# Performance work log

Measured on AMD Instinct MI355X. Metric: run time of the kernel, lower is better.

## Reference

```python
import jax, jax.numpy as jnp
import numpy as np

B, D, C, N = 8, 49, 512, 12
BN_EPS = 1e-5
SCALE = (C // 2) ** -0.5


def bn_train(x, axes):
    # training-mode batchnorm, gamma=1 beta=0 (per bn_init / default init)
    m = jnp.mean(x, axis=axes, keepdims=True)
    v = jnp.var(x, axis=axes, keepdims=True)
    return (x - m) * jax.lax.rsqrt(v + BN_EPS)


def l2norm(x):
    n = jnp.linalg.norm(x, axis=-1, keepdims=True)
    return x / jnp.maximum(n, 1e-12)


def cross_attn(y, xkv, wq, bq, wk, bk, wv, bv):
    q = y @ wq + bq
    k = xkv @ wk + bk
    v = xkv @ wv + bv
    a = jax.nn.softmax(jnp.einsum('...ik,...jk->...ij', q, k) * SCALE, axis=-1)
    return a @ v


def _gnn_layer(xv, ed, wa, wb, we, wu, wv):
    # incidence-matrix einsums reduce to repeat (end-gather) / tile (start-gather)
    res = xv
    agg = jnp.repeat(xv @ wa, N, axis=1) + jnp.tile(xv @ wb, (1, N, 1)) + ed @ we
    ed = ed + jax.nn.relu(bn_train(agg, (0, 2)))
    e = jax.nn.sigmoid(ed).reshape(-1, N, N, C)
    e = jax.nn.softmax(e, axis=2).reshape(-1, N * N, C)
    uj = jnp.tile(xv @ wv, (1, N, 1))
    msg = (e * uj).reshape(-1, N, N, C).sum(axis=2) / N  # scatter via end.T
    xv = jax.nn.relu(res + bn_train(xv @ wu + msg, (0, 2)))
    return xv, ed


def setup_inputs() -> dict:
    ks = iter(jax.random.split(jax.random.key(0), 64))

    def nrm(shape, scale=0.02):
        return jax.random.normal(next(ks), shape, dtype=jnp.float32) * scale

    g = float(np.sqrt(2.0 / C))
    inp = {'x': jax.random.normal(next(ks), (B, D, C), dtype=jnp.float32)}
    inp['Wc'] = nrm((N, C, C))
    inp['bc'] = nrm((N, C), 0.01)
    for p in ('fam', 'arm'):
        inp[p + '_wq'] = nrm((C, C // 2))
        inp[p + '_bq'] = nrm((C // 2,), 0.01)
        inp[p + '_wk'] = nrm((C, C // 2))
        inp[p + '_bk'] = nrm((C // 2,), 0.01)
        inp[p + '_wv'] = nrm((C, C))
        inp[p + '_bv'] = nrm((C,), 0.01)
    inp['ep_w'] = nrm((C, C))
    inp['ep_b'] = nrm((C,), 0.01)
    for nm in ('g_wa1', 'g_wb1', 'g_we1', 'g_wu1', 'g_wv1',
               'g_wa2', 'g_wb2', 'g_we2', 'g_wu2', 'g_wv2'):
        inp[nm] = nrm((C, C), g)
    inp['sc'] = nrm((N, C), float(np.sqrt(6.0 / (N + C))))
    inp['efc_w'] = nrm((C, 4), float(np.sqrt(6.0 / (C + 4))))
    inp['efc_b'] = nrm((4,), 0.01)
    return inp


def reference(x, Wc, bc,
              fam_wq, fam_bq, fam_wk, fam_bk, fam_wv, fam_bv,
              arm_wq, arm_bq, arm_wk, arm_bk, arm_wv, arm_bv,
              ep_w, ep_b,
              g_wa1, g_wb1, g_we1, g_wu1, g_wv1,
              g_wa2, g_wb2, g_we2, g_wu2, g_wv2,
              sc, efc_w, efc_b):
    b = x.shape[0]
    # per-class LinearBlocks (fc -> BN -> ReLU), vectorized over classes
    h = jnp.einsum('bdc,nco->bndo', x, Wc) + bc[None, :, None, :]
    f_u = jax.nn.relu(bn_train(h, (0, 2)))          # (b, N, D, C)
    f_v = f_u.mean(axis=2)                           # (b, N, C)
    # GEM edge extractor
    gf = jnp.broadcast_to(x[:, None], (b, N, D, C))
    feat = cross_attn(f_u, gf, fam_wq, fam_bq, fam_wk, fam_bk, fam_wv, fam_bv)
    feat_end = jnp.repeat(feat, N, axis=1)           # (b, N*N, D, C): edge (i,j) -> node i
    feat_start = jnp.tile(feat, (1, N, 1, 1))        # edge (i,j) -> node j
    feat = cross_attn(feat_start, feat_end, arm_wq, arm_bq, arm_wk, arm_bk, arm_wv, arm_bv)
    f_e = bn_train(feat @ ep_w + ep_b, (0, 2, 3)).mean(axis=2)  # (b, N*N, C)
    # cosine-similarity adjacency mask (detached), digraph-normalized
    si = l2norm(jax.lax.stop_gradient(f_v))
    adj = jnp.einsum('bik,bjk->bij', si, si)
    dis = jnp.sum(adj, axis=-1) ** -0.5
    mask = (adj * dis[:, :, None] * dis[:, None, :]).reshape(b, N * N, 1)
    f_e = f_e * mask
    # two GNN message-passing layers
    f_v, f_e = _gnn_layer(f_v, f_e, g_wa1, g_wb1, g_we1, g_wu1, g_wv1)
    f_v, f_e = _gnn_layer(f_v, f_e, g_wa2, g_wb2, g_we2, g_wu2, g_wv2)
    # cosine classifier + edge fc
    scn = l2norm(jax.nn.relu(sc))
    cl = jnp.sum(l2norm(f_v) * scn[None], axis=-1)   # (b, N)
    cl_edge = f_e @ efc_w + efc_b                    # (b, N*N, 4)
    return cl, cl_edge
```

## Files before the change

kernel.cpp:

```cpp
#include <hip/hip_runtime.h>
#include <math.h>

namespace {

constexpr int B = 8, D = 49, C = 512, N = 12, H = 256, E = 144;
constexpr int M_BD  = B * D;
constexpr int M_BND = B * N * D;
constexpr float BN_EPS = 1e-5f;
constexpr float ATT_SCALE = 0.0625f;

typedef __attribute__((ext_vector_type(4))) float  floatx4;
typedef __attribute__((ext_vector_type(8))) short  shortx8;

__device__ inline unsigned short f2bf(float f) {
  unsigned u = __float_as_uint(f);
  return (unsigned short)((u + 0x7fffu + ((u >> 16) & 1u)) >> 16);
}
__device__ inline float bf2f(unsigned short u) {
  return __uint_as_float(((unsigned)u) << 16);
}

__device__ inline void gload16(const unsigned short* g, unsigned short* l) {
  __builtin_amdgcn_global_load_lds(
      (const __attribute__((address_space(1))) void*)g,
      (__attribute__((address_space(3))) void*)l, 16, 0, 0);
}

struct TCJobs {
  const float* src[28];
  unsigned short* dst[28];
  int nn[28];
};

__global__ __launch_bounds__(256)
void tcast_k(TCJobs jobs,
             const float* __restrict__ x, unsigned short* __restrict__ xb,
             const float* __restrict__ awv, unsigned short* __restrict__ armwvb,
             const float* __restrict__ bk, const float* __restrict__ bv,
             const float* __restrict__ bq2, const float* __restrict__ bk2,
             const float* __restrict__ arm_bv, const float* __restrict__ epw,
             const float* __restrict__ epb,
             float* __restrict__ kvbias, float* __restrict__ qkvbias)
{
  const int z = blockIdx.z;
  const int tid = threadIdx.x;
  if (z == 28) {
    int idx = (blockIdx.y * 16 + blockIdx.x) * 256 + tid;
    const int n1 = M_BD * C / 8;
    const int n2 = n1 + C * C / 8;
    if (idx < n1) {
      int i8 = idx * 8;
      float4 a = *reinterpret_cast<const float4*>(x + i8);
      float4 b = *reinterpret_cast<const float4*>(x + i8 + 4);
      shortx8 o;
      o[0]=(short)f2bf(a.x); o[1]=(short)f2bf(a.y); o[2]=(short)f2bf(a.z); o[3]=(short)f2bf(a.w);
      o[4]=(short)f2bf(b.x); o[5]=(short)f2bf(b.y); o[6]=(short)f2bf(b.z); o[7]=(short)f2bf(b.w);
      *reinterpret_cast<shortx8*>(xb + i8) = o;
    } else if (idx < n2) {
      int i8 = (idx - n1) * 8;
      float4 a = *reinterpret_cast<const float4*>(awv + i8);
      float4 b = *reinterpret_cast<const float4*>(awv + i8 + 4);
      shortx8 o;
      o[0]=(short)f2bf(a.x); o[1]=(short)f2bf(a.y); o[2]=(short)f2bf(a.z); o[3]=(short)f2bf(a.w);
      o[4]=(short)f2bf(b.x); o[5]=(short)f2bf(b.y); o[6]=(short)f2bf(b.z); o[7]=(short)f2bf(b.w);
      *reinterpret_cast<shortx8*>(armwvb + i8) = o;
    } else if (idx >= 58112 && idx < 58624) {
      int c = idx - 58112;
      float s = epb[c];
      for (int k = 0; k < C; ++k) s = fmaf(arm_bv[k], epw[k * C + c], s);
      qkvbias[512 + c] = s;
    }
    if (idx < 256) { kvbias[idx] = bk[idx]; qkvbias[idx] = bq2[idx]; qkvbias[256 + idx] = bk2[idx]; }
    if (idx < 512) kvbias[256 + idx] = bv[idx];
    return;
  }
  const float* src = jobs.src[z];
  unsigned short* dst = jobs.dst[z];
  const int Nn = jobs.nn[z];
  const int tx = blockIdx.x, ty = blockIdx.y;
  if (tx * 32 >= Nn) return;
  __shared__ float t[32][33];
  const int lr = tid >> 5, lc = tid & 31;
#pragma unroll
  for (int p = 0; p < 4; ++p) {
    int k = ty * 32 + p * 8 + lr;
    t[p * 8 + lr][lc] = src[(long long)k * Nn + tx * 32 + lc];
  }
  __syncthreads();
#pragma unroll
  for (int p = 0; p < 4; ++p) {
    int n = tx * 32 + p * 8 + lr;
    dst[(long long)n * 512 + ty * 32 + lc] = f2bf(t[lc][p * 8 + lr]);
  }
}

__device__ __forceinline__
void gemm64_body(const void* __restrict__ Ain, const unsigned short* __restrict__ Bt,
                 const float* __restrict__ bp, float* __restrict__ co,
                 unsigned short* __restrict__ cb,
                 int M, int Nn, int K, int lda, int ldb, int ldc, int abf,
                 int bx, int by)
{
  const float* Af = abf ? nullptr : (const float*)Ain;
  const unsigned short* Ab = abf ? (const unsigned short*)Ain : nullptr;

  __shared__ short As[64 * 72];
  __shared__ short Bs[64 * 72];

  const int tid = threadIdx.x;
  const int row0 = bx * 64, col0 = by * 64;
  const int wid = tid >> 6, lane = tid & 63;
  const int wr = wid >> 1, wc = wid & 1;
  const int lr = lane & 15, lg = lane >> 4;

  floatx4 acc00 = {0.f,0.f,0.f,0.f}, acc01 = {0.f,0.f,0.f,0.f};
  floatx4 acc10 = {0.f,0.f,0.f,0.f}, acc11 = {0.f,0.f,0.f,0.f};

  const int r = tid >> 2, seg = tid & 3;
  const int gr = row0 + r, gn = col0 + r;
  short* aw = &As[r * 72 + seg * 16];
  short* bw = &Bs[r * 72 + seg * 16];
  const shortx8 zz = {0,0,0,0,0,0,0,0};

  for (int k0 = 0; k0 < K; k0 += 64) {
    shortx8 w0, w1;
    if (gr < M) {
      if (abf) {
        const shortx8* ap = reinterpret_cast<const shortx8*>(Ab + (long long)gr * lda + seg * 16 + k0);
        w0 = ap[0]; w1 = ap[1];
      } else {
        const float4* ap = reinterpret_cast<const float4*>(Af + (long long)gr * lda + seg * 16 + k0);
        float4 fa0 = ap[0], fa1 = ap[1], fa2 = ap[2], fa3 = ap[3];
        w0[0]=(short)f2bf(fa0.x); w0[1]=(short)f2bf(fa0.y); w0[2]=(short)f2bf(fa0.z); w0[3]=(short)f2bf(fa0.w);
        w0[4]=(short)f2bf(fa1.x); w0[5]=(short)f2bf(fa1.y); w0[6]=(short)f2bf(fa1.z); w0[7]=(short)f2bf(fa1.w);
        w1[0]=(short)f2bf(fa2.x); w1[1]=(short)f2bf(fa2.y); w1[2]=(short)f2bf(fa2.z); w1[3]=(short)f2bf(fa2.w);
        w1[4]=(short)f2bf(fa3.x); w1[5]=(short)f2bf(fa3.y); w1[6]=(short)f2bf(fa3.z); w1[7]=(short)f2bf(fa3.w);
      }
    } else { w0 = zz; w1 = zz; }
    const shortx8* bp8 = reinterpret_cast<const shortx8*>(Bt + (long long)gn * ldb + seg * 16 + k0);
    shortx8 b0v = bp8[0];
    shortx8 b1v = bp8[1];

    __syncthreads();
    *reinterpret_cast<shortx8*>(aw)     = w0;
    *reinterpret_cast<shortx8*>(aw + 8) = w1;
    *reinterpret_cast<shortx8*>(bw)     = b0v;
    *reinterpret_cast<shortx8*>(bw + 8) = b1v;
    __syncthreads();

#pragma unroll
    for (int kt = 0; kt < 2; ++kt) {
      shortx8 a0 = *reinterpret_cast<const shortx8*>(&As[(wr*32      + lr) * 72 + kt*32 + lg*8]);
      shortx8 a1 = *reinterpret_cast<const shortx8*>(&As[(wr*32 + 16 + lr) * 72 + kt*32 + lg*8]);
      shortx8 bb0 = *reinterpret_cast<const shortx8*>(&Bs[(wc*32      + lr) * 72 + kt*32 + lg*8]);
      shortx8 bb1 = *reinterpret_cast<const shortx8*>(&Bs[(wc*32 + 16 + lr) * 72 + kt*32 + lg*8]);
      acc00 = __builtin_amdgcn_mfma_f32_16x16x32_bf16(a0, bb0, acc00, 0, 0, 0);
      acc01 = __builtin_amdgcn_mfma_f32_16x16x32_bf16(a0, bb1, acc01, 0, 0, 0);
      acc10 = __builtin_amdgcn_mfma_f32_16x16x32_bf16(a1, bb0, acc10, 0, 0, 0);
      acc11 = __builtin_amdgcn_mfma_f32_16x16x32_bf16(a1, bb1, acc11, 0, 0, 0);
    }
  }

  const int colA = col0 + wc * 32 + lr;
  const int colB = colA + 16;
  const bool okA = colA < Nn, okB = colB < Nn;
  const float biasA = (bp && okA) ? bp[colA] : 0.f;
  const float biasB = (bp && okB) ? bp[colB] : 0.f;
  const int rb0 = row0 + wr * 32 + lg * 4;
  const int rb1 = rb0 + 16;
#pragma unroll
  for (int jj = 0; jj < 4; ++jj) {
    int ra = rb0 + jj, rb = rb1 + jj;
    float v00 = acc00[jj] + biasA, v01 = acc01[jj] + biasB;
    float v10 = acc10[jj] + biasA, v11 = acc11[jj] + biasB;
    if (ra < M) {
      if (co) { if (okA) co[(long long)ra * ldc + colA] = v00;
                if (okB) co[(long long)ra * ldc + colB] = v01; }
      if (cb) { if (okA) cb[(long long)ra * ldc + colA] = f2bf(v00);
                if (okB) cb[(long long)ra * ldc + colB] = f2bf(v01); }
    }
    if (rb < M) {
      if (co) { if (okA) co[(long long)rb * ldc + colA] = v10;
                if (okB) co[(long long)rb * ldc + colB] = v11; }
      if (cb) { if (okA) cb[(long long)rb * ldc + colA] = f2bf(v10);
                if (okB) cb[(long long)rb * ldc + colB] = f2bf(v11); }
    }
  }
}

__global__ __launch_bounds__(256)
void gemm_mfma(const void* __restrict__ Ain, const unsigned short* __restrict__ Bt,
               const float* __restrict__ bias, float* __restrict__ Co,
               unsigned short* __restrict__ Cb,
               int M, int Nn, int K, int lda, int ldb, int ldc, int abf,
               long long sA, long long sB, long long sBias, long long sC)
{
  const int z = blockIdx.z;
  const void* A = abf ? (const void*)((const unsigned short*)Ain + z * sA)
                      : (const void*)((const float*)Ain + z * sA);
  gemm64_body(A, Bt + z * sB, bias ? bias + z * sBias : nullptr,
              Co ? Co + z * sC : nullptr, Cb ? Cb + z * sC : nullptr,
              M, Nn, K, lda, ldb, ldc, abf, blockIdx.x, blockIdx.y);
}

struct GJob {
  const void* A; const unsigned short* B; const float* bias;
  float* Co; unsigned short* Cb;
  int M, Nn, K, lda, ldb, ldc, abf, tx;
};
struct GJobs { GJob j[3]; int ends[3]; int n; };

__global__ __launch_bounds__(256)
void gemm_jobs(GJobs js)
{
  const int bid = blockIdx.x;
#pragma unroll
  for (int q = 0; q < 3; ++q) {
    if (q < js.n && bid < js.ends[q]) {
      int start = q ? js.ends[q - 1] : 0;
      int local = bid - start;
      const GJob& J = js.j[q];
      gemm64_body(J.A, J.B, J.bias, J.Co, J.Cb,
                  J.M, J.Nn, J.K, J.lda, J.ldb, J.ldc, J.abf,
                  local % J.tx, local / J.tx);
      return;
    }
  }
}

__device__ __forceinline__
void g128_body(const unsigned short* __restrict__ Ab, const unsigned short* __restrict__ Bt,
               const float* __restrict__ bp, float* __restrict__ co,
               unsigned short* __restrict__ cb, float* __restrict__ psb, float* __restrict__ pqb,
               int M, int Nn, int K, int lda, int ldb, int ldc, int bx, int by)
{
  __shared__ unsigned short As[128 * 64];
  __shared__ unsigned short Bs[128 * 64];

  const int tid = threadIdx.x;
  const int row0 = bx * 128, col0 = by * 128;
  const int wid = tid >> 6, lane = tid & 63;
  const int wr = wid >> 1, wc = wid & 1;
  const int lr = lane & 15, lg = lane >> 4;

  floatx4 acc[4][4];
#pragma unroll
  for (int mf = 0; mf < 4; ++mf)
#pragma unroll
    for (int nf = 0; nf < 4; ++nf) acc[mf][nf] = floatx4{0.f,0.f,0.f,0.f};

  const int rsub = tid >> 3;
  const int csub = (tid & 7) * 8;

  for (int k0 = 0; k0 < K; k0 += 64) {
    __syncthreads();
#pragma unroll
    for (int it = 0; it < 4; ++it) {
      int r = it * 32 + rsub;
      gload16(Ab + (long long)(row0 + r) * lda + k0 + csub, As + it * 2048 + tid * 8);
      gload16(Bt + (long long)(col0 + r) * ldb + k0 + csub, Bs + it * 2048 + tid * 8);
    }
    __syncthreads();

#pragma unroll
    for (int kt = 0; kt < 2; ++kt) {
      shortx8 af[4], bf[4];
#pragma unroll
      for (int mf = 0; mf < 4; ++mf)
        af[mf] = *reinterpret_cast<const shortx8*>(&As[(wr*64 + mf*16 + lr) * 64 + kt*32 + lg*8]);
#pragma unroll
      for (int nf = 0; nf < 4; ++nf)
        bf[nf] = *reinterpret_cast<const shortx8*>(&Bs[(wc*64 + nf*16 + lr) * 64 + kt*32 + lg*8]);
#pragma unroll
      for (int mf = 0; mf < 4; ++mf)
#pragma unroll
        for (int nf = 0; nf < 4; ++nf)
          acc[mf][nf] = __builtin_amdgcn_mfma_f32_16x16x32_bf16(af[mf], bf[nf], acc[mf][nf], 0, 0, 0);
    }
  }

#pragma unroll
  for (int nf = 0; nf < 4; ++nf) {
    const int col = col0 + wc * 64 + nf * 16 + lr;
    if (col >= Nn) continue;
    const float bv = bp ? bp[col] : 0.f;
#pragma unroll
    for (int mf = 0; mf < 4; ++mf) {
      const int rbase = row0 + wr * 64 + mf * 16 + lg * 4;
#pragma unroll
      for (int jj = 0; jj < 4; ++jj) {
        int row = rbase + jj;
        if (row >= M) continue;
        float v = acc[mf][nf][jj] + bv;
        if (co) co[(long long)row * ldc + col] = v;
        if (cb) cb[(long long)row * ldc + col] = f2bf(v);
      }
    }
  }

  if (psb) {
    __syncthreads();
    float* sb = (float*)As;
    sb[tid] = 0.f;
    __syncthreads();
#pragma unroll
    for (int nf = 0; nf < 4; ++nf) {
      const int lcol = wc * 64 + nf * 16 + lr;
      const int col = col0 + lcol;
      float s = 0.f, q = 0.f;
      if (col < Nn) {
        const float bv = bp ? bp[col] : 0.f;
#pragma unroll
        for (int mf = 0; mf < 4; ++mf) {
          const int rbase = row0 + wr * 64 + mf * 16 + lg * 4;
#pragma unroll
          for (int jj = 0; jj < 4; ++jj) {
            if (rbase + jj < M) { float v = acc[mf][nf][jj] + bv; s += v; q += v * v; }
          }
        }
      }
      atomicAdd(&sb[lcol], s);
      atomicAdd(&sb[128 + lcol], q);
    }
    __syncthreads();
    if (tid < 128) {
      psb[col0 + tid] = sb[tid];
      pqb[col0 + tid] = sb[128 + tid];
    }
  }
}

__global__ __launch_bounds__(256)
void gemm128g(const unsigned short* __restrict__ Ab, const unsigned short* __restrict__ Bt,
              const float* __restrict__ bias, float* __restrict__ Co,
              unsigned short* __restrict__ Cb, float* __restrict__ ps, float* __restrict__ pq,
              int M, int Nn, int K, int lda, int ldb, int ldc,
              long long sA, long long sB, long long sBias, long long sC)
{
  const int z = blockIdx.z;
  long long so = ((long long)blockIdx.x * gridDim.z + z) * ldc;
  g128_body(Ab + z * sA, Bt + z * sB, bias ? bias + z * sBias : nullptr,
            Co ? Co + z * sC : nullptr, Cb ? Cb + z * sC : nullptr,
            ps ? ps + so : nullptr, pq ? pq + so : nullptr,
            M, Nn, K, lda, ldb, ldc, blockIdx.x, blockIdx.y);
}

__global__ __launch_bounds__(256)
void scgm_k(const unsigned short* __restrict__ qkvfe, float* __restrict__ Sc,
            float* __restrict__ Gm)
{
  const int bid = blockIdx.x;
  if (bid < 200) {
    int z = bid / 25, rem = bid % 25;
    g128_body(qkvfe + (long long)z * 588 * 1024, qkvfe + 256 + (long long)z * 588 * 1024,
              nullptr, Sc + (long long)z * 588 * 588, nullptr, nullptr, nullptr,
              588, 588, H, 1024, 1024, 588, rem % 5, rem / 5);
  } else {
    int z = bid - 200;
    const unsigned short* vp = qkvfe + 512 + (long long)z * 49 * 1024;
    gemm64_body(vp, vp, nullptr, Gm + (long long)z * 2401, nullptr,
                D, D, C, 1024, 1024, D, 1, 0, 0);
  }
}

__global__ __launch_bounds__(256)
void fu_fv(const float* __restrict__ h, const float* __restrict__ ps,
           const float* __restrict__ pq, unsigned short* __restrict__ fub,
           float* __restrict__ fv)
{
  const int bid = blockIdx.x;
  const int b = bid / N, n = bid % N;
  const int c = blockIdx.y * 256 + threadIdx.x;
  const int idx = n * C + c;
  float s = 0.f, q = 0.f;
#pragma unroll
  for (int sl = 0; sl < 4; ++sl) { s += ps[sl * (N * C) + idx]; q += pq[sl * (N * C) + idx]; }
  float m = s / (float)M_BD;
  float rv = rsqrtf(q / (float)M_BD - m * m + BN_EPS);
  float acc = 0.f;
  for (int d = 0; d < D; ++d) {
    float v = h[((long long)n * M_BD + b * D + d) * C + c];
    v = fmaxf((v - m) * rv, 0.f);
    fub[((long long)bid * D + d) * C + c] = f2bf(v);
    acc += v;
  }
  fv[(long long)bid * C + c] = acc * (1.0f / (float)D);
}

__global__ __launch_bounds__(256)
void softvxt_k(const float* __restrict__ Sf, unsigned short* __restrict__ Ppb,
               const unsigned short* __restrict__ kvx, unsigned short* __restrict__ vxtb,
               const float* __restrict__ fv, float* __restrict__ maskp)
{
  const int tid = threadIdx.x;
  if (blockIdx.x < 19) {
    int row = blockIdx.x * 256 + tid;
    if (row >= M_BND) return;
    const float* p = Sf + (long long)row * 49;
    float v[49];
    float m = -1e30f;
#pragma unroll
    for (int j = 0; j < 49; ++j) { v[j] = p[j] * ATT_SCALE; m = fmaxf(m, v[j]); }
    float s = 0.f;
#pragma unroll
    for (int j = 0; j < 49; ++j) { v[j] = __expf(v[j] - m); s += v[j]; }
    float inv = 1.f / s;
    unsigned short* o = Ppb + (long long)row * 64;
#pragma unroll
    for (int j = 0; j < 49; ++j) o[j] = f2bf(v[j] * inv);
#pragma unroll
    for (int j = 49; j < 64; ++j) o[j] = 0;
    return;
  }
  if (blockIdx.x < 83) {
    const int i = blockIdx.x - 19;
    const int b = i >> 3, cc = i & 7;
    __shared__ unsigned short t[49][65];
    for (int idx = tid; idx < 49 * 64; idx += 256) {
      int rr = idx >> 6, k = idx & 63;
      t[rr][k] = kvx[(long long)(b * 49 + rr) * 768 + 256 + cc * 64 + k];
    }
    __syncthreads();
    for (int idx = tid; idx < 64 * 64; idx += 256) {
      int n = idx >> 6, kk = idx & 63;
      vxtb[((long long)b * 512 + cc * 64 + n) * 64 + kk] = (kk < 49) ? t[kk][n] : (unsigned short)0;
    }
    return;
  }
  const int b = blockIdx.x - 83;
  __shared__ float fl[N][C];
  __shared__ float adj[N][N];
  __shared__ float nrm[N];
  __shared__ float dis[N];
  for (int idx = tid; idx < N * C; idx += 256)
    fl[idx / C][idx % C] = fv[(long long)b * N * C + idx];
  __syncthreads();
  if (tid < N * N) {
    int i = tid / N, j = tid % N;
    float s = 0.f;
    for (int k = 0; k < C; ++k) s += fl[i][k] * fl[j][k];
    adj[i][j] = s;
  }
  __syncthreads();
  if (tid < N) nrm[tid] = fmaxf(sqrtf(adj[tid][tid]), 1e-12f);
  __syncthreads();
  if (tid < N * N) {
    int i = tid / N, j = tid % N;
    adj[i][j] = adj[i][j] / (nrm[i] * nrm[j]);
  }
  __syncthreads();
  if (tid < N) {
    float s = 0.f;
    for (int j = 0; j < N; ++j) s += adj[tid][j];
    dis[tid] = rsqrtf(s);
  }
  __syncthreads();
  if (tid < N * N) {
    int i = tid / N, j = tid % N;
    maskp[b * E + tid] = adj[i][j] * dis[i] * dis[j];
  }
}

__global__ __launch_bounds__(256)
void edge_finish(const float* __restrict__ Sc, const float* __restrict__ G,
                 const unsigned short* __restrict__ qkvfe,
                 float* __restrict__ S1, float* __restrict__ eS)
{
  const int bid = blockIdx.x;
  const int b = bid / E, e = bid % E;
  const int i = e / N, j = e % N;
  const float* Scb = Sc + (long long)b * 588 * 588 + (long long)(j * 49) * 588 + i * 49;
  const float* Gp  = G + (long long)(b * N + i) * 2401;
  const unsigned short* Vp = qkvfe + (long long)(b * N + i) * D * 1024 + 512;

  __shared__ float aT[49][53];
  __shared__ float g[49][53];
  __shared__ unsigned short abT[64][72];
  __shared__ float ws[52];
  __shared__ float r0[4], r1[4];
  const int tid = threadIdx.x;
  const int wid = tid >> 6, lane = tid & 63;
  const int lr = lane & 15, lg = lane >> 4;

  for (int idx = tid; idx < 49 * 49; idx += 256) {
    int di = idx / 49, dj = idx - di * 49;
    aT[dj][di] = Scb[di * 588 + dj] * ATT_SCALE;
    g[di][dj] = Gp[idx];
  }
  __syncthreads();
  if (tid < D) {
    float m = -1e30f;
    for (int jj = 0; jj < D; ++jj) m = fmaxf(m, aT[jj][tid]);
    float s = 0.f;
    for (int jj = 0; jj < D; ++jj) { float ev = __expf(aT[jj][tid] - m); aT[jj][tid] = ev; s += ev; }
    float inv = 1.f / s;
    for (int jj = 0; jj < D; ++jj) aT[jj][tid] *= inv;
  }
  __syncthreads();
  for (int idx = tid; idx < 64 * 64; idx += 256) {
    int dj = idx >> 6, di = idx & 63;
    float v = (dj < D && di < D) ? aT[dj][di] : 0.f;
    abT[dj][di] = f2bf(v);
  }
  if (tid < D) {
    float s = 0.f;
    for (int di = 0; di < D; ++di) s += aT[tid][di];
    ws[tid] = s;
  }
  __syncthreads();

  floatx4 acc[4];
#pragma unroll
  for (int tk = 0; tk < 4; ++tk) acc[tk] = floatx4{0.f,0.f,0.f,0.f};
  shortx8 af0 = *reinterpret_cast<const shortx8*>(&abT[wid * 16 + lr][lg * 8]);
  shortx8 af1 = *reinterpret_cast<const shortx8*>(&abT[wid * 16 + lr][32 + lg * 8]);
#pragma unroll
  for (int tk = 0; tk < 4; ++tk) {
    shortx8 bf0v = *reinterpret_cast<const shortx8*>(&abT[tk * 16 + lr][lg * 8]);
    shortx8 bf1v = *reinterpret_cast<const shortx8*>(&abT[tk * 16 + lr][32 + lg * 8]);
    acc[tk] = __builtin_amdgcn_mfma_f32_16x16x32_bf16(af0, bf0v, acc[tk], 0, 0, 0);
    acc[tk] = __builtin_amdgcn_mfma_f32_16x16x32_bf16(af1, bf1v, acc[tk], 0, 0, 0);
  }
  float st2 = 0.f;
#pragma unroll
  for (int tk = 0; tk < 4; ++tk) {
    int kcol = tk * 16 + lr;
#pragma unroll
    for (int rg = 0; rg < 4; ++rg) {
      int jrow = wid * 16 + lg * 4 + rg;
      if (jrow < D && kcol < D) st2 = fmaf(acc[tk][rg], g[jrow][kcol], st2);
    }
  }

  const unsigned* Vp32 = reinterpret_cast<const unsigned*>(Vp);
  float s1a = 0.f, s1b = 0.f;
  for (int dk = 0; dk < D; ++dk) {
    unsigned u = Vp32[dk * 512 + tid];
    float w = ws[dk];
    s1a = fmaf(w, bf2f((unsigned short)(u & 0xffffu)), s1a);
    s1b = fmaf(w, bf2f((unsigned short)(u >> 16)), s1b);
  }
  S1[(long long)bid * C + 2 * tid]     = s1a;
  S1[(long long)bid * C + 2 * tid + 1] = s1b;
  float st = s1a + s1b;

  for (int off = 32; off; off >>= 1) { st += __shfl_down(st, off); st2 += __shfl_down(st2, off); }
  if (lane == 0) { r0[wid] = st; r1[wid] = st2; }
  __syncthreads();
  if (tid == 0) {
    eS[bid * 2 + 0] = r0[0] + r0[1] + r0[2] + r0[3];
    eS[bid * 2 + 1] = r1[0] + r1[1] + r1[2] + r1[3];
  }
}

__global__ __launch_bounds__(256)
void fe_k(const float* __restrict__ S1, const float* __restrict__ eS,
          const float* __restrict__ maskp, float* __restrict__ fe)
{
  __shared__ float csh[3];
  long long idx0 = (long long)blockIdx.x * 256;
  long long be = idx0 / C;
  int e = (int)(be % E);
  if (threadIdx.x == 0) {
    float s = 0.f, q = 0.f;
    for (int b = 0; b < B; ++b) { s += eS[(b * E + e) * 2]; q += eS[(b * E + e) * 2 + 1]; }
    const float inv = 1.f / (float)(B * D * C);
    float m = s * inv;
    csh[0] = m;
    csh[1] = rsqrtf(q * inv - m * m + BN_EPS);
    csh[2] = maskp[be];
  }
  __syncthreads();
  long long idx = idx0 + threadIdx.x;
  fe[idx] = (S1[idx] * (1.0f / (float)D) - csh[0]) * csh[1] * csh[2];
}

__global__ __launch_bounds__(256)
void agg_stats(const float* __restrict__ ABUV, const float* __restrict__ EW,
               float* __restrict__ mu_e, float* __restrict__ rs_e)
{
  const int e = blockIdx.x;
  const int i = e / N, j = e % N;
  const int tid = threadIdx.x;
  float s = 0.f, q = 0.f;
  for (int idx = tid; idx < B * C; idx += 256) {
    int b = idx >> 9, c = idx & 511;
    float v = ABUV[(long long)(b * N + i) * 2048 + c]
            + ABUV[(long long)(b * N + j) * 2048 + 512 + c]
            + EW[((long long)b * E + e) * C + c];
    s += v; q += v * v;
  }
  for (int off = 32; off; off >>= 1) { s += __shfl_down(s, off); q += __shfl_down(q, off); }
  __shared__ float r0[4], r1[4];
  int wid = tid >> 6, lane = tid & 63;
  if (lane == 0) { r0[wid] = s; r1[wid] = q; }
  __syncthreads();
  if (tid == 0) {
    float ss = r0[0] + r0[1] + r0[2] + r0[3];
    float qq = r1[0] + r1[1] + r1[2] + r1[3];
    float m = ss / (float)(B * C);
    mu_e[e] = m;
    rs_e[e] = rsqrtf(qq / (float)(B * C) - m * m + BN_EPS);
  }
}

__global__ __launch_bounds__(256)
void edmsg_k(float* __restrict__ fe, const float* __restrict__ ABUV,
             const float* __restrict__ EW, const float* __restrict__ mu_e,
             const float* __restrict__ rs_e, float* __restrict__ pre,
             float* __restrict__ nps, float* __restrict__ npq)
{
  const int bid = blockIdx.x;
  const int b = bid / N, i = bid % N;
  const int tid = threadIdx.x;
  float ls = 0.f, lq = 0.f;
  for (int c = tid; c < C; c += 256) {
    float ai = ABUV[(long long)(b * N + i) * 2048 + c];
    float sv[N];
    float m = -1e30f;
#pragma unroll
    for (int jn = 0; jn < N; ++jn) {
      int e = i * N + jn;
      float v = ai + ABUV[(long long)(b * N + jn) * 2048 + 512 + c]
              + EW[((long long)b * E + e) * C + c];
      v = (v - mu_e[e]) * rs_e[e];
      float ed = fe[((long long)b * E + e) * C + c] + fmaxf(v, 0.f);
      fe[((long long)b * E + e) * C + c] = ed;
      float sg = 1.f / (1.f + __expf(-ed));
      sv[jn] = sg; m = fmaxf(m, sg);
    }
    float sum = 0.f;
#pragma unroll
    for (int jn = 0; jn < N; ++jn) { float ev = __expf(sv[jn] - m); sv[jn] = ev; sum += ev; }
    float acc = 0.f;
#pragma unroll
    for (int jn = 0; jn < N; ++jn)
      acc = fmaf(sv[jn], ABUV[(long long)(b * N + jn) * 2048 + 1536 + c], acc);
    acc /= (sum * (float)N);
    float pv = ABUV[(long long)bid * 2048 + 1024 + c] + acc;
    pre[(long long)bid * C + c] = pv;
    ls += pv; lq += pv * pv;
  }
  for (int off = 32; off; off >>= 1) { ls += __shfl_down(ls, off); lq += __shfl_down(lq, off); }
  __shared__ float r0[4], r1[4];
  int wid = tid >> 6, lane = tid & 63;
  if (lane == 0) { r0[wid] = ls; r1[wid] = lq; }
  __syncthreads();
  if (tid == 0) {
    nps[i * B + b] = r0[0] + r0[1] + r0[2] + r0[3];
    npq[i * B + b] = r1[0] + r1[1] + r1[2] + r1[3];
  }
}

__global__ void xv_update(float* __restrict__ xv, const float* __restrict__ pre,
                          const float* __restrict__ nps, const float* __restrict__ npq)
{
  long long idx = (long long)blockIdx.x * 256 + threadIdx.x;
  if (idx >= (long long)B * N * C) return;
  int i = (int)((idx / C) % N);
  float s = 0.f, q = 0.f;
#pragma unroll
  for (int bb = 0; bb < B; ++bb) { s += nps[i * B + bb]; q += npq[i * B + bb]; }
  float mu = s * (1.f / (float)(B * C));
  float rs = rsqrtf(q * (1.f / (float)(B * C)) - mu * mu + BN_EPS);
  float v = xv[idx] + (pre[idx] - mu) * rs;
  xv[idx] = fmaxf(v, 0.f);
}

__global__ __launch_bounds__(256)
void out_k(const float* __restrict__ xv, const float* __restrict__ sc,
           const float* __restrict__ ed, const float* __restrict__ w,
           const float* __restrict__ bias, float* __restrict__ out)
{
  const int bid = blockIdx.x;
  const int tid = threadIdx.x;
  int wid = tid >> 6, lane = tid & 63;
  if (bid < B * N) {
    const int b = bid / N, i = bid % N;
    float sxx = 0.f, sss = 0.f, sxs = 0.f;
    for (int c = tid; c < C; c += 256) {
      float xvv = xv[(long long)(b * N + i) * C + c];
      float scv = fmaxf(sc[i * C + c], 0.f);
      sxx += xvv * xvv; sss += scv * scv; sxs += xvv * scv;
    }
    for (int off = 32; off; off >>= 1) {
      sxx += __shfl_down(sxx, off);
      sss += __shfl_down(sss, off);
      sxs += __shfl_down(sxs, off);
    }
    __shared__ float r0[4], r1[4], r2[4];
    if (lane == 0) { r0[wid] = sxx; r1[wid] = sss; r2[wid] = sxs; }
    __syncthreads();
    if (tid == 0) {
      float a = r0[0] + r0[1] + r0[2] + r0[3];
      float s = r1[0] + r1[1] + r1[2] + r1[3];
      float p = r2[0] + r2[1] + r2[2] + r2[3];
      float nx = fmaxf(sqrtf(a), 1e-12f);
      float ns = fmaxf(sqrtf(s), 1e-12f);
      out[b * N + i] = p / (nx * ns);
    }
  } else {
    const int eb = bid - B * N;
    float a0 = 0, a1 = 0, a2 = 0, a3 = 0;
    for (int c = tid; c < C; c += 256) {
      float v = ed[(long long)eb * C + c];
      a0 = fmaf(v, w[c * 4 + 0], a0);
      a1 = fmaf(v, w[c * 4 + 1], a1);
      a2 = fmaf(v, w[c * 4 + 2], a2);
      a3 = fmaf(v, w[c * 4 + 3], a3);
    }
    for (int off = 32; off; off >>= 1) {
      a0 += __shfl_down(a0, off);
      a1 += __shfl_down(a1, off);
      a2 += __shfl_down(a2, off);
      a3 += __shfl_down(a3, off);
    }
    __shared__ float r[4][4];
    if (lane == 0) { r[wid][0] = a0; r[wid][1] = a1; r[wid][2] = a2; r[wid][3] = a3; }
    __syncthreads();
    if (tid < 4) {
      float s = r[0][tid] + r[1][tid] + r[2][tid] + r[3][tid];
      out[B * N + eb * 4 + tid] = s + bias[tid];
    }
  }
}

}

extern "C" void kernel_launch(void* const* d_in, const int* in_sizes, int n_in,
                              void* d_out, int out_size, void* d_ws, size_t ws_size,
                              hipStream_t stream)
{
  (void)in_sizes; (void)n_in; (void)out_size; (void)ws_size;
  const float* x      = (const float*)d_in[0];
  const float* Wc     = (const float*)d_in[1];
  const float* bc     = (const float*)d_in[2];
  const float* fam_wq = (const float*)d_in[3];
  const float* fam_bq = (const float*)d_in[4];
  const float* fam_wk = (const float*)d_in[5];
  const float* fam_bk = (const float*)d_in[6];
  const float* fam_wv = (const float*)d_in[7];
  const float* fam_bv = (const float*)d_in[8];
  const float* arm_wq = (const float*)d_in[9];
  const float* arm_bq = (const float*)d_in[10];
  const float* arm_wk = (const float*)d_in[11];
  const float* arm_bk = (const float*)d_in[12];
  const float* arm_wv = (const float*)d_in[13];
  const float* arm_bv = (const float*)d_in[14];
  const float* ep_w   = (const float*)d_in[15];
  const float* ep_b   = (const float*)d_in[16];
  const float* gw[10] = {
    (const float*)d_in[17], (const float*)d_in[18], (const float*)d_in[19],
    (const float*)d_in[20], (const float*)d_in[21],
    (const float*)d_in[22], (const float*)d_in[23], (const float*)d_in[24],
    (const float*)d_in[25], (const float*)d_in[26]};
  const float* sc     = (const float*)d_in[27];
  const float* efc_w  = (const float*)d_in[28];
  const float* efc_b  = (const float*)d_in[29];
  float* out = (float*)d_out;

  char* wsb = (char*)d_ws;
  size_t off = 0;
  auto allocf = [&](size_t n) { float* p = (float*)(wsb + off); off += ((n * 4 + 255) / 256) * 256; return p; };
  auto allocu = [&](size_t n) { unsigned short* p = (unsigned short*)(wsb + off); off += ((n * 2 + 255) / 256) * 256; return p; };

  float* region_a = allocf(2766336);
  float* h_t = region_a;
  float* Sc  = region_a;

  float* bnp_s = allocf(24576);
  float* bnp_q = allocf(24576);
  float* f_v   = allocf(49152);
  float* Sf    = allocf(230496);
  float* Gm    = allocf(230496);
  float* S1    = allocf(589824);
  float* fe    = allocf(589824);
  float* EW    = allocf(589824);
  float* eS    = allocf(2304);
  float* mask  = allocf(1152);
  float* ABUV  = allocf(196608);
  float* pre   = allocf(49152);
  float* mu_e  = allocf(144);
  float* rs_e  = allocf(144);
  float* nps   = allocf(96);
  float* npq   = allocf(96);
  float* kvbias  = allocf(768);
  float* qkvbias = allocf(1024);

  unsigned short* Wct    = allocu(3145728);
  unsigned short* famqt  = allocu(131072);
  unsigned short* kvwt   = allocu(393216);
  unsigned short* qkw2t  = allocu(524288);
  unsigned short* epwt   = allocu(262144);
  unsigned short* armwvb = allocu(262144);
  unsigned short* wet0   = allocu(262144);
  unsigned short* wet1   = allocu(262144);
  unsigned short* ABUVt0 = allocu(1048576);
  unsigned short* ABUVt1 = allocu(1048576);
  unsigned short* xb     = allocu(262144);
  unsigned short* fub    = allocu(2408448);
  unsigned short* q1b    = allocu(1204224);
  unsigned short* kxvx_b = allocu(350208);
  unsigned short* Ppb    = allocu(301056);
  unsigned short* vxtb   = allocu(262144);
  unsigned short* featb  = allocu(2424832);
  unsigned short* qkvfe  = allocu(4915200);

  dim3 blk(256);

  TCJobs tj{};
  int jn = 0;
  for (int n = 0; n < 12; ++n) { tj.src[jn] = Wc + (size_t)n * C * C; tj.dst[jn] = Wct + (size_t)n * C * C; tj.nn[jn] = C; ++jn; }
  tj.src[jn] = fam_wq; tj.dst[jn] = famqt;             tj.nn[jn] = H; ++jn;
  tj.src[jn] = fam_wk; tj.dst[jn] = kvwt;              tj.nn[jn] = H; ++jn;
  tj.src[jn] = fam_wv; tj.dst[jn] = kvwt + 256 * 512;  tj.nn[jn] = C; ++jn;
  tj.src[jn] = arm_wq; tj.dst[jn] = qkw2t;             tj.nn[jn] = H; ++jn;
  tj.src[jn] = arm_wk; tj.dst[jn] = qkw2t + 256 * 512; tj.nn[jn] = H; ++jn;
  tj.src[jn] = ep_w;   tj.dst[jn] = epwt;              tj.nn[jn] = C; ++jn;
  tj.src[jn] = gw[2];  tj.dst[jn] = wet0;              tj.nn[jn] = C; ++jn;
  tj.src[jn] = gw[7];  tj.dst[jn] = wet1;              tj.nn[jn] = C; ++jn;
  tj.src[jn] = gw[0];  tj.dst[jn] = ABUVt0;               tj.nn[jn] = C; ++jn;
  tj.src[jn] = gw[1];  tj.dst[jn] = ABUVt0 + 1 * C * C;   tj.nn[jn] = C; ++jn;
  tj.src[jn] = gw[3];  tj.dst[jn] = ABUVt0 + 2 * C * C;   tj.nn[jn] = C; ++jn;
  tj.src[jn] = gw[4];  tj.dst[jn] = ABUVt0 + 3 * C * C;   tj.nn[jn] = C; ++jn;
  tj.src[jn] = gw[5];  tj.dst[jn] = ABUVt1;               tj.nn[jn] = C; ++jn;
  tj.src[jn] = gw[6];  tj.dst[jn] = ABUVt1 + 1 * C * C;   tj.nn[jn] = C; ++jn;
  tj.src[jn] = gw[8];  tj.dst[jn] = ABUVt1 + 2 * C * C;   tj.nn[jn] = C; ++jn;
  tj.src[jn] = gw[9];  tj.dst[jn] = ABUVt1 + 3 * C * C;   tj.nn[jn] = C; ++jn;
  tcast_k<<<dim3(16, 16, 29), blk, 0, stream>>>(tj, x, xb, arm_wv, armwvb,
      fam_bk, fam_bv, arm_bq, arm_bk, arm_bv, ep_w, ep_b, kvbias, qkvbias);

  gemm128g<<<dim3(4, 4, 12), blk, 0, stream>>>(xb, Wct, bc, h_t, nullptr, bnp_s, bnp_q,
      M_BD, C, C, C, C, C, 0LL, (long long)C * C, (long long)C, (long long)M_BD * C);
  fu_fv<<<dim3(B * N, 2), blk, 0, stream>>>(h_t, bnp_s, bnp_q, fub, f_v);

  {
    GJobs js{};
    js.j[0] = {fub,  famqt,  fam_bq, nullptr, q1b,            M_BND, H,   C, C, C, H,   1, 74};
    js.j[1] = {xb,   kvwt,   kvbias, nullptr, kxvx_b,         M_BD,  768, C, C, C, 768, 1, 7};
    js.j[2] = {epwt, armwvb, nullptr, nullptr, qkw2t + 512 * 512, C,  C,   C, C, C, C,   1, 8};
    js.ends[0] = 296; js.ends[1] = 380; js.ends[2] = 444; js.n = 3;
    gemm_jobs<<<dim3(444), blk, 0, stream>>>(js);
  }
  gemm_mfma<<<dim3(10, 1, 8), blk, 0, stream>>>(q1b, kxvx_b, nullptr, Sf, nullptr,
      588, 49, H, H, 768, 49, 1, 588LL * 256, 49LL * 768, 0LL, 588LL * 49);
  softvxt_k<<<dim3(91), blk, 0, stream>>>(Sf, Ppb, kxvx_b, vxtb, f_v, mask);
  gemm_mfma<<<dim3(10, 8, 8), blk, 0, stream>>>(Ppb, vxtb, nullptr, nullptr, featb,
      588, C, 64, 64, 64, C, 1, 588LL * 64, 512LL * 64, 0LL, 588LL * 512);

  gemm128g<<<dim3(37, 8, 1), blk, 0, stream>>>(featb, qkw2t, qkvbias, nullptr, qkvfe,
      nullptr, nullptr, M_BND, 1024, C, C, C, 1024, 0, 0, 0, 0);

  scgm_k<<<dim3(296), blk, 0, stream>>>(qkvfe, Sc, Gm);

  edge_finish<<<dim3(B * E), blk, 0, stream>>>(Sc, Gm, qkvfe, S1, eS);
  fe_k<<<dim3(2304), blk, 0, stream>>>(S1, eS, mask, fe);

  for (int L = 0; L < 2; ++L) {
    const unsigned short* ABUVt = L ? ABUVt1 : ABUVt0;
    const unsigned short* wet   = L ? wet1 : wet0;
    {
      GJobs js{};
      js.j[0] = {f_v, ABUVt, nullptr, ABUV, nullptr, B * N, 2048, C, C, C, 2048, 0, 2};
      js.j[1] = {fe,  wet,   nullptr, EW,   nullptr, B * E, C,    C, C, C, C,    0, 18};
      js.ends[0] = 64; js.ends[1] = 208; js.ends[2] = 208; js.n = 2;
      gemm_jobs<<<dim3(208), blk, 0, stream>>>(js);
    }
    agg_stats<<<dim3(E), blk, 0, stream>>>(ABUV, EW, mu_e, rs_e);
    edmsg_k<<<dim3(B * N), blk, 0, stream>>>(fe, ABUV, EW, mu_e, rs_e, pre, nps, npq);
    xv_update<<<dim3((B * N * C + 255) / 256), blk, 0, stream>>>(f_v, pre, nps, npq);
  }

  out_k<<<dim3(B * N + B * E), blk, 0, stream>>>(f_v, sc, fe, efc_w, efc_b, out);
}
```

Measured before the change: 213.1 us.

## Fuse QK score GEMM into edge_finish, split edmsg grid, fold final xv update into out_k

The big batched QK^T score GEMM that wrote a 588x588 fp32 Sc matrix per batch is removed. Each edge_finish block now computes its own 49x49 Q·K block with bf16 MFMA from swizzled LDS tiles, which avoids the global round trip of Sc. The Gram matrix is now computed by a separate batched gemm_mfma launch. edmsg_k is split across two channel halves to double its block count, with per-half partial statistics. The last layer's xv_update is folded into out_k, removing one launch. The trade-off is that each edge block recomputes a small GEMM in place of reading precomputed scores.

Result: slower. 231.5 us (+8.6%).

```diff
diff --git a/kernel.cpp b/kernel.cpp
--- a/kernel.cpp
+++ b/kernel.cpp
@@ -346,24 +346,6 @@
 }
 
 __global__ __launch_bounds__(256)
-void scgm_k(const unsigned short* __restrict__ qkvfe, float* __restrict__ Sc,
-            float* __restrict__ Gm)
-{
-  const int bid = blockIdx.x;
-  if (bid < 200) {
-    int z = bid / 25, rem = bid % 25;
-    g128_body(qkvfe + (long long)z * 588 * 1024, qkvfe + 256 + (long long)z * 588 * 1024,
-              nullptr, Sc + (long long)z * 588 * 588, nullptr, nullptr, nullptr,
-              588, 588, H, 1024, 1024, 588, rem % 5, rem / 5);
-  } else {
-    int z = bid - 200;
-    const unsigned short* vp = qkvfe + 512 + (long long)z * 49 * 1024;
-    gemm64_body(vp, vp, nullptr, Gm + (long long)z * 2401, nullptr,
-                D, D, C, 1024, 1024, D, 1, 0, 0);
-  }
-}
-
-__global__ __launch_bounds__(256)
 void fu_fv(const float* __restrict__ h, const float* __restrict__ ps,
            const float* __restrict__ pq, unsigned short* __restrict__ fub,
            float* __restrict__ fv)
@@ -462,29 +444,71 @@
 }
 
 __global__ __launch_bounds__(256)
-void edge_finish(const float* __restrict__ Sc, const float* __restrict__ G,
-                 const unsigned short* __restrict__ qkvfe,
+void edge_finish(const unsigned short* __restrict__ qkvfe, const float* __restrict__ G,
                  float* __restrict__ S1, float* __restrict__ eS)
 {
   const int bid = blockIdx.x;
   const int b = bid / E, e = bid % E;
   const int i = e / N, j = e % N;
-  const float* Scb = Sc + (long long)b * 588 * 588 + (long long)(j * 49) * 588 + i * 49;
-  const float* Gp  = G + (long long)(b * N + i) * 2401;
+  const unsigned short* Qp = qkvfe + (long long)(b * N + j) * D * 1024;
+  const unsigned short* Kp = qkvfe + (long long)(b * N + i) * D * 1024 + 256;
   const unsigned short* Vp = qkvfe + (long long)(b * N + i) * D * 1024 + 512;
-
-  __shared__ float aT[49][53];
-  __shared__ float g[49][53];
-  __shared__ unsigned short abT[64][72];
+  const float* Gp = G + (long long)(b * N + i) * 2401;
+
+  __shared__ char smem_raw[33024] __attribute__((aligned(16)));
+  unsigned short* sq = (unsigned short*)smem_raw;
+  unsigned short* sk = sq + 64 * 128;
+  float (*aT)[53] = (float (*)[53])smem_raw;
+  float (*g)[53]  = (float (*)[53])(smem_raw + 10400);
+  unsigned short (*abT)[72] = (unsigned short (*)[72])(smem_raw + 20800);
   __shared__ float ws[52];
   __shared__ float r0[4], r1[4];
+
   const int tid = threadIdx.x;
   const int wid = tid >> 6, lane = tid & 63;
   const int lr = lane & 15, lg = lane >> 4;
 
+  floatx4 qk[4];
+#pragma unroll
+  for (int f = 0; f < 4; ++f) qk[f] = floatx4{0.f,0.f,0.f,0.f};
+  for (int p = 0; p < 2; ++p) {
+    __syncthreads();
+    for (int idx = tid; idx < 49 * 16; idx += 256) {
+      int row = idx >> 4, seg = idx & 15;
+      int dsti = row * 128 + ((seg ^ (row & 7)) << 3);
+      *reinterpret_cast<shortx8*>(sq + dsti) =
+          *reinterpret_cast<const shortx8*>(Qp + row * 1024 + p * 128 + seg * 8);
+      *reinterpret_cast<shortx8*>(sk + dsti) =
+          *reinterpret_cast<const shortx8*>(Kp + row * 1024 + p * 128 + seg * 8);
+    }
+    __syncthreads();
+#pragma unroll
+    for (int kt = 0; kt < 4; ++kt) {
+      const int arow = wid * 16 + lr;
+      shortx8 a = *reinterpret_cast<const shortx8*>(
+          sk + arow * 128 + (((kt * 4 + lg) ^ (arow & 7)) << 3));
+#pragma unroll
+      for (int f = 0; f < 4; ++f) {
+        const int brow = f * 16 + lr;
+        shortx8 bb = *reinterpret_cast<const shortx8*>(
+            sq + brow * 128 + (((kt * 4 + lg) ^ (brow & 7)) << 3));
+        qk[f] = __builtin_amdgcn_mfma_f32_16x16x32_bf16(a, bb, qk[f], 0, 0, 0);
+      }
+    }
+  }
+  __syncthreads();
+
+#pragma unroll
+  for (int f = 0; f < 4; ++f) {
+#pragma unroll
+    for (int jj = 0; jj < 4; ++jj) {
+      int dj = wid * 16 + lg * 4 + jj;
+      int di = f * 16 + lr;
+      if (dj < D && di < D) aT[dj][di] = qk[f][jj] * ATT_SCALE;
+    }
+  }
   for (int idx = tid; idx < 49 * 49; idx += 256) {
     int di = idx / 49, dj = idx - di * 49;
-    aT[dj][di] = Scb[di * 588 + dj] * ATT_SCALE;
     g[di][dj] = Gp[idx];
   }
   __syncthreads();
@@ -612,43 +636,43 @@
 {
   const int bid = blockIdx.x;
   const int b = bid / N, i = bid % N;
+  const int half = blockIdx.y;
   const int tid = threadIdx.x;
-  float ls = 0.f, lq = 0.f;
-  for (int c = tid; c < C; c += 256) {
-    float ai = ABUV[(long long)(b * N + i) * 2048 + c];
-    float sv[N];
-    float m = -1e30f;
-#pragma unroll
-    for (int jn = 0; jn < N; ++jn) {
-      int e = i * N + jn;
-      float v = ai + ABUV[(long long)(b * N + jn) * 2048 + 512 + c]
-              + EW[((long long)b * E + e) * C + c];
-      v = (v - mu_e[e]) * rs_e[e];
-      float ed = fe[((long long)b * E + e) * C + c] + fmaxf(v, 0.f);
-      fe[((long long)b * E + e) * C + c] = ed;
-      float sg = 1.f / (1.f + __expf(-ed));
-      sv[jn] = sg; m = fmaxf(m, sg);
-    }
-    float sum = 0.f;
-#pragma unroll
-    for (int jn = 0; jn < N; ++jn) { float ev = __expf(sv[jn] - m); sv[jn] = ev; sum += ev; }
-    float acc = 0.f;
-#pragma unroll
-    for (int jn = 0; jn < N; ++jn)
-      acc = fmaf(sv[jn], ABUV[(long long)(b * N + jn) * 2048 + 1536 + c], acc);
-    acc /= (sum * (float)N);
-    float pv = ABUV[(long long)bid * 2048 + 1024 + c] + acc;
-    pre[(long long)bid * C + c] = pv;
-    ls += pv; lq += pv * pv;
-  }
+  const int c = half * 256 + tid;
+
+  float ai = ABUV[(long long)(b * N + i) * 2048 + c];
+  float sv[N];
+  float m = -1e30f;
+#pragma unroll
+  for (int jn = 0; jn < N; ++jn) {
+    int e = i * N + jn;
+    float v = ai + ABUV[(long long)(b * N + jn) * 2048 + 512 + c]
+            + EW[((long long)b * E + e) * C + c];
+    v = (v - mu_e[e]) * rs_e[e];
+    float ed = fe[((long long)b * E + e) * C + c] + fmaxf(v, 0.f);
+    fe[((long long)b * E + e) * C + c] = ed;
+    float sg = 1.f / (1.f + __expf(-ed));
+    sv[jn] = sg; m = fmaxf(m, sg);
+  }
+  float sum = 0.f;
+#pragma unroll
+  for (int jn = 0; jn < N; ++jn) { float ev = __expf(sv[jn] - m); sv[jn] = ev; sum += ev; }
+  float acc = 0.f;
+#pragma unroll
+  for (int jn = 0; jn < N; ++jn)
+    acc = fmaf(sv[jn], ABUV[(long long)(b * N + jn) * 2048 + 1536 + c], acc);
+  acc /= (sum * (float)N);
+  float pv = ABUV[(long long)bid * 2048 + 1024 + c] + acc;
+  pre[(long long)bid * C + c] = pv;
+  float ls = pv, lq = pv * pv;
   for (int off = 32; off; off >>= 1) { ls += __shfl_down(ls, off); lq += __shfl_down(lq, off); }
   __shared__ float r0[4], r1[4];
   int wid = tid >> 6, lane = tid & 63;
   if (lane == 0) { r0[wid] = ls; r1[wid] = lq; }
   __syncthreads();
   if (tid == 0) {
-    nps[i * B + b] = r0[0] + r0[1] + r0[2] + r0[3];
-    npq[i * B + b] = r1[0] + r1[1] + r1[2] + r1[3];
+    nps[(i * B + b) * 2 + half] = r0[0] + r0[1] + r0[2] + r0[3];
+    npq[(i * B + b) * 2 + half] = r1[0] + r1[1] + r1[2] + r1[3];
   }
 }
 
@@ -660,7 +684,7 @@
   int i = (int)((idx / C) % N);
   float s = 0.f, q = 0.f;
 #pragma unroll
-  for (int bb = 0; bb < B; ++bb) { s += nps[i * B + bb]; q += npq[i * B + bb]; }
+  for (int t = 0; t < B * 2; ++t) { s += nps[i * B * 2 + t]; q += npq[i * B * 2 + t]; }
   float mu = s * (1.f / (float)(B * C));
   float rs = rsqrtf(q * (1.f / (float)(B * C)) - mu * mu + BN_EPS);
   float v = xv[idx] + (pre[idx] - mu) * rs;
@@ -668,7 +692,9 @@
 }
 
 __global__ __launch_bounds__(256)
-void out_k(const float* __restrict__ xv, const float* __restrict__ sc,
+void out_k(const float* __restrict__ xv, const float* __restrict__ pre,
+           const float* __restrict__ nps, const float* __restrict__ npq,
+           const float* __restrict__ sc,
            const float* __restrict__ ed, const float* __restrict__ w,
            const float* __restrict__ bias, float* __restrict__ out)
 {
@@ -677,9 +703,14 @@
   int wid = tid >> 6, lane = tid & 63;
   if (bid < B * N) {
     const int b = bid / N, i = bid % N;
+    float s = 0.f, q = 0.f;
+#pragma unroll
+    for (int t = 0; t < B * 2; ++t) { s += nps[i * B * 2 + t]; q += npq[i * B * 2 + t]; }
+    float mu = s * (1.f / (float)(B * C));
+    float rs = rsqrtf(q * (1.f / (float)(B * C)) - mu * mu + BN_EPS);
     float sxx = 0.f, sss = 0.f, sxs = 0.f;
     for (int c = tid; c < C; c += 256) {
-      float xvv = xv[(long long)(b * N + i) * C + c];
+      float xvv = fmaxf(xv[(long long)bid * C + c] + (pre[(long long)bid * C + c] - mu) * rs, 0.f);
       float scv = fmaxf(sc[i * C + c], 0.f);
       sxx += xvv * xvv; sss += scv * scv; sxs += xvv * scv;
     }
@@ -693,10 +724,10 @@
     __syncthreads();
     if (tid == 0) {
       float a = r0[0] + r0[1] + r0[2] + r0[3];
-      float s = r1[0] + r1[1] + r1[2] + r1[3];
+      float ss = r1[0] + r1[1] + r1[2] + r1[3];
       float p = r2[0] + r2[1] + r2[2] + r2[3];
       float nx = fmaxf(sqrtf(a), 1e-12f);
-      float ns = fmaxf(sqrtf(s), 1e-12f);
+      float ns = fmaxf(sqrtf(ss), 1e-12f);
       out[b * N + i] = p / (nx * ns);
     }
   } else {
@@ -719,8 +750,8 @@
     if (lane == 0) { r[wid][0] = a0; r[wid][1] = a1; r[wid][2] = a2; r[wid][3] = a3; }
     __syncthreads();
     if (tid < 4) {
-      float s = r[0][tid] + r[1][tid] + r[2][tid] + r[3][tid];
-      out[B * N + eb * 4 + tid] = s + bias[tid];
+      float sr = r[0][tid] + r[1][tid] + r[2][tid] + r[3][tid];
+      out[B * N + eb * 4 + tid] = sr + bias[tid];
     }
   }
 }
@@ -764,10 +795,7 @@
   auto allocf = [&](size_t n) { float* p = (float*)(wsb + off); off += ((n * 4 + 255) / 256) * 256; return p; };
   auto allocu = [&](size_t n) { unsigned short* p = (unsigned short*)(wsb + off); off += ((n * 2 + 255) / 256) * 256; return p; };
 
-  float* region_a = allocf(2766336);
-  float* h_t = region_a;
-  float* Sc  = region_a;
-
+  float* h_t   = allocf(2408448);
   float* bnp_s = allocf(24576);
   float* bnp_q = allocf(24576);
   float* f_v   = allocf(49152);
@@ -782,8 +810,8 @@
   float* pre   = allocf(49152);
   float* mu_e  = allocf(144);
   float* rs_e  = allocf(144);
-  float* nps   = allocf(96);
-  float* npq   = allocf(96);
+  float* nps   = allocf(192);
+  float* npq   = allocf(192);
   float* kvbias  = allocf(768);
   float* qkvbias = allocf(1024);
 
@@ -851,9 +879,10 @@
   gemm128g<<<dim3(37, 8, 1), blk, 0, stream>>>(featb, qkw2t, qkvbias, nullptr, qkvfe,
       nullptr, nullptr, M_BND, 1024, C, C, C, 1024, 0, 0, 0, 0);
 
-  scgm_k<<<dim3(296), blk, 0, stream>>>(qkvfe, Sc, Gm);
-
-  edge_finish<<<dim3(B * E), blk, 0, stream>>>(Sc, Gm, qkvfe, S1, eS);
+  gemm_mfma<<<dim3(1, 1, 96), blk, 0, stream>>>(qkvfe + 512, qkvfe + 512, nullptr, Gm, nullptr,
+      D, D, C, 1024, 1024, D, 1, 49LL * 1024, 49LL * 1024, 0LL, 49LL * 49);
+
+  edge_finish<<<dim3(B * E), blk, 0, stream>>>(qkvfe, Gm, S1, eS);
   fe_k<<<dim3(2304), blk, 0, stream>>>(S1, eS, mask, fe);
 
   for (int L = 0; L < 2; ++L) {
@@ -867,9 +896,10 @@
       gemm_jobs<<<dim3(208), blk, 0, stream>>>(js);
     }
     agg_stats<<<dim3(E), blk, 0, stream>>>(ABUV, EW, mu_e, rs_e);
-    edmsg_k<<<dim3(B * N), blk, 0, stream>>>(fe, ABUV, EW, mu_e, rs_e, pre, nps, npq);
-    xv_update<<<dim3((B * N * C + 255) / 256), blk, 0, stream>>>(f_v, pre, nps, npq);
-  }
-
-  out_k<<<dim3(B * N + B * E), blk, 0, stream>>>(f_v, sc, fe, efc_w, efc_b, out);
-}
+    edmsg_k<<<dim3(B * N, 2), blk, 0, stream>>>(fe, ABUV, EW, mu_e, rs_e, pre, nps, npq);
+    if (L == 0)
+      xv_update<<<dim3((B * N * C + 255) / 256), blk, 0, stream>>>(f_v, pre, nps, npq);
+  }
+
+  out_k<<<dim3(B * N + B * E), blk, 0, stream>>>(f_v, pre, nps, npq, sc, fe, efc_w, efc_b, out);
+}
```
